# Kernel tuning notes

Hardware: AMD Instinct MI355X
Metric: run time of the kernel (lower is better)

The kernel has to match this reference:

```python
import jax, jax.numpy as jnp
import numpy as np

N = 50000        # nodes
E = 800000       # edges (before self loops)
F_IN = 128
HID = 32         # per-head out channels (hidden_size)
H = 4            # heads
NCLS = 10
NG = 64          # graphs in batch
SLOPE = 0.2      # GATConv default negative_slope


def setup_inputs() -> dict:
    key = jax.random.key(0)
    ks = jax.random.split(key, 32)

    def p(k, shape, fan_in):
        s = 1.0 / np.sqrt(fan_in)
        return jax.random.uniform(k, shape, jnp.float32, -s, s)

    inp = {
        'x': jax.random.normal(ks[0], (N, F_IN), jnp.float32),
        'edge_index': jax.random.randint(ks[1], (2, E), 0, N),
        'batch': jnp.sort(jax.random.randint(ks[2], (N,), 0, NG)),
        'enc1_w': p(ks[3], (F_IN, 128), F_IN), 'enc1_b': p(ks[4], (128,), F_IN),
        'enc2_w': p(ks[5], (128, 256), 128),   'enc2_b': p(ks[6], (256,), 128),
        'lin1_w': p(ks[7], (HID, NCLS), HID),  'lin1_b': p(ks[8], (NCLS,), HID),
    }
    dims_in = [256, HID, HID, HID]
    for i in range(4):
        kk = jax.random.split(ks[9 + i], 4)
        din = dims_in[i]
        inp[f'g{i+1}_w'] = p(kk[0], (din, H * HID), din)
        inp[f'g{i+1}_as'] = p(kk[1], (H, HID), HID)
        inp[f'g{i+1}_ad'] = p(kk[2], (H, HID), HID)
        inp[f'g{i+1}_b'] = p(kk[3], (HID,), HID)
    return inp


def gat_layer(h_in, w, a_s, a_d, b, src, dst):
    # h: [N,H,C] per-head projected features
    h = (h_in @ w).reshape(N, H, HID)
    sc_s = jnp.sum(h * a_s, axis=-1)                 # [N,H] att_src . x
    sc_d = jnp.sum(h * a_d, axis=-1)                 # [N,H] att_dst . x
    e = jax.nn.leaky_relu(sc_s[src] + sc_d[dst], SLOPE)   # [Etot,H]
    m = jax.ops.segment_max(e, dst, num_segments=N)
    m = jnp.where(jnp.isfinite(m), m, 0.0)
    al = jnp.exp(e - m[dst])
    den = jax.ops.segment_sum(al, dst, num_segments=N)
    al = al / jnp.maximum(den[dst], 1e-16)           # segment softmax over in-edges
    msg = h[src] * al[:, :, None]                    # [Etot,H,C]
    out = jax.ops.segment_sum(msg, dst, num_segments=N)  # [N,H,C]
    return out.mean(axis=1) + b                      # concat=False -> head mean + bias


def reference(x, edge_index, batch,
              enc1_w, enc1_b, enc2_w, enc2_b, lin1_w, lin1_b,
              g1_w, g1_as, g1_ad, g1_b,
              g2_w, g2_as, g2_ad, g2_b,
              g3_w, g3_as, g3_ad, g3_b,
              g4_w, g4_as, g4_ad, g4_b):
    loops = jnp.arange(N)
    src = jnp.concatenate([edge_index[0], loops])    # PyG add_self_loops=True
    dst = jnp.concatenate([edge_index[1], loops])
    h = x @ enc1_w + enc1_b                          # no activation in original
    h = h @ enc2_w + enc2_b
    h = jax.nn.elu(gat_layer(h, g1_w, g1_as, g1_ad, g1_b, src, dst))
    h = jax.nn.elu(gat_layer(h, g2_w, g2_as, g2_ad, g2_b, src, dst))
    h = jax.nn.elu(gat_layer(h, g3_w, g3_as, g3_ad, g3_b, src, dst))
    h = jax.nn.elu(gat_layer(h, g4_w, g4_as, g4_ad, g4_b, src, dst))
    sums = jax.ops.segment_sum(h, batch, num_segments=NG)
    cnt = jax.ops.segment_sum(jnp.ones((N,), h.dtype), batch, num_segments=NG)
    pooled = sums / jnp.maximum(cnt, 1.0)[:, None]   # global_mean_pool
    return pooled @ lin1_w + lin1_b                  # dropout off at inference
```

## Files before the change

kernel.cpp:

```cpp
#include <hip/hip_runtime.h>
#include <hip/hip_fp16.h>
#include <math.h>

#define NNODES 50000
#define NEDGES 800000
#define ETOT   (NEDGES + NNODES)
#define HIDC   32
#define NGRAPH 64
#define NCLS   10
#define SLOPE  0.2f
#define SCAN_BLOCKS ((NNODES + 255) / 256)

typedef _Float16 h8 __attribute__((ext_vector_type(8)));
typedef float f32x4 __attribute__((ext_vector_type(4)));

__device__ __forceinline__ float lrelu(float v) { return v > 0.f ? v : SLOPE * v; }

__global__ void hist_kernel(const int* __restrict__ ei, int* __restrict__ deg,
                            int* __restrict__ epos) {
  int base = blockIdx.x * 1024 + threadIdx.x;
  #pragma unroll
  for (int u = 0; u < 4; ++u) {
    int e = base + u * 256;
    if (e < NEDGES) {
      int d = ei[NEDGES + e];
      epos[e] = atomicAdd(&deg[d], 1);
    }
  }
}

__global__ __launch_bounds__(256)
void scan_block_kernel(const int* __restrict__ deg, int* __restrict__ row_start,
                       int* __restrict__ bsum) {
  __shared__ int wsum[4];
  int i = blockIdx.x * 256 + threadIdx.x;
  int v = (i < NNODES) ? (deg[i] + 1) : 0;
  int lane = threadIdx.x & 63, w = threadIdx.x >> 6;
  int x = v;
  #pragma unroll
  for (int d = 1; d < 64; d <<= 1) {
    int y = __shfl_up(x, d);
    if (lane >= d) x += y;
  }
  if (lane == 63) wsum[w] = x;
  __syncthreads();
  int woff = 0;
  #pragma unroll
  for (int j = 0; j < 4; ++j) if (j < w) woff += wsum[j];
  int incl = x + woff;
  if (i < NNODES) row_start[i] = incl - v;
  if (threadIdx.x == 255) bsum[blockIdx.x] = incl;
}

__global__ __launch_bounds__(256)
void scan_add_kernel(const int* __restrict__ bsum, int* __restrict__ row_start,
                     int* __restrict__ col_src) {
  __shared__ int wsum[4];
  int tid = threadIdx.x;
  int v = (tid < blockIdx.x) ? bsum[tid] : 0;
  int lane = tid & 63, w = tid >> 6;
  #pragma unroll
  for (int d = 32; d >= 1; d >>= 1) v += __shfl_xor(v, d);
  if (lane == 0) wsum[w] = v;
  __syncthreads();
  int boff = wsum[0] + wsum[1] + wsum[2] + wsum[3];
  int i = blockIdx.x * 256 + tid;
  if (i < NNODES) {
    int rs = row_start[i] + boff;
    row_start[i] = rs;
    col_src[rs] = i;
  }
  if (i == 0) row_start[NNODES] = ETOT;
}

__global__ void scatter_kernel(const int* __restrict__ ei, const int* __restrict__ row_start,
                               const int* __restrict__ epos, int* __restrict__ col_src) {
  int base = blockIdx.x * 1024 + threadIdx.x;
  #pragma unroll
  for (int u = 0; u < 4; ++u) {
    int e = base + u * 256;
    if (e < NEDGES) {
      int s = ei[e], d = ei[NEDGES + e];
      col_src[row_start[d] + 1 + epos[e]] = s;
    }
  }
}

__device__ void gemm_tile(const float* __restrict__ A, const float* __restrict__ B,
                          float* __restrict__ C, int K, int N, int row0, int col0,
                          float (*As)[68], float (*Bs)[68]) {
  int tid = threadIdx.x;
  int tx = tid & 15, ty = tid >> 4;
  float acc[4][4] = {};
  for (int k0 = 0; k0 < K; k0 += 32) {
    #pragma unroll
    for (int i = 0; i < 8; ++i) {
      int idx = tid + i * 256;
      int r = idx >> 5, c = idx & 31;
      As[c][r] = A[(size_t)(row0 + r) * K + k0 + c];
    }
    #pragma unroll
    for (int i = 0; i < 8; ++i) {
      int idx = tid + i * 256;
      int r = idx >> 6, c = idx & 63;
      Bs[r][c] = B[(size_t)(k0 + r) * N + col0 + c];
    }
    __syncthreads();
    #pragma unroll
    for (int k = 0; k < 32; ++k) {
      float a4[4], b4[4];
      #pragma unroll
      for (int i = 0; i < 4; ++i) a4[i] = As[k][ty * 4 + i];
      #pragma unroll
      for (int j = 0; j < 4; ++j) b4[j] = Bs[k][tx * 4 + j];
      #pragma unroll
      for (int i = 0; i < 4; ++i)
        #pragma unroll
        for (int j = 0; j < 4; ++j)
          acc[i][j] = fmaf(a4[i], b4[j], acc[i][j]);
    }
    __syncthreads();
  }
  #pragma unroll
  for (int i = 0; i < 4; ++i)
    #pragma unroll
    for (int j = 0; j < 4; ++j)
      C[(size_t)(row0 + ty * 4 + i) * N + col0 + tx * 4 + j] = acc[i][j];
}

__global__ __launch_bounds__(256)
void wprep1(const float* __restrict__ enc1_w, const float* __restrict__ enc2_w,
            const float* __restrict__ enc1_b, const float* __restrict__ enc2_b,
            const float* __restrict__ gw1, const float* __restrict__ gas1, const float* __restrict__ gad1,
            const float* __restrict__ gw2, const float* __restrict__ gas2, const float* __restrict__ gad2,
            const float* __restrict__ gw3, const float* __restrict__ gas3, const float* __restrict__ gad3,
            float* __restrict__ T1, float* __restrict__ b2c,
            float* __restrict__ Ws2, float* __restrict__ Ws3, float* __restrict__ Ws4,
            float* __restrict__ pooled) {
  __shared__ float As[32][68];
  __shared__ float Bs[32][68];
  int b = blockIdx.x, tid = threadIdx.x;
  if (b < 8) {
    gemm_tile(enc1_w, enc2_w, T1, 128, 256, (b >> 2) * 64, (b & 3) * 64, As, Bs);
  } else if (b == 8) {
    float acc = enc2_b[tid];
    for (int k = 0; k < 128; ++k) acc = fmaf(enc1_b[k], enc2_w[k * 256 + tid], acc);
    b2c[tid] = acc;
    for (int i = tid; i < NGRAPH * HIDC + NGRAPH; i += 256) pooled[i] = 0.f;
  } else {
    const float* W   = (b == 9) ? gw1  : (b == 10) ? gw2  : gw3;
    const float* as_ = (b == 9) ? gas1 : (b == 10) ? gas2 : gas3;
    const float* ad_ = (b == 9) ? gad1 : (b == 10) ? gad2 : gad3;
    float* Ws        = (b == 9) ? Ws2  : (b == 10) ? Ws3  : Ws4;
    int r = tid >> 3, j = tid & 7, h = j & 3;
    const float* a = (j < 4) ? as_ : ad_;
    float s = 0.f;
    for (int c = 0; c < 32; ++c) s = fmaf(W[r * 128 + h * 32 + c], a[h * 32 + c], s);
    Ws[tid] = s;
  }
}

__global__ __launch_bounds__(256)
void wprep2(const float* __restrict__ T1, const float* __restrict__ gw0,
            const float* __restrict__ b2c, float* __restrict__ Wc, float* __restrict__ bc) {
  __shared__ float As[32][68];
  __shared__ float Bs[32][68];
  int b = blockIdx.x, tid = threadIdx.x;
  if (b < 4) {
    gemm_tile(T1, gw0, Wc, 256, 128, (b >> 1) * 64, (b & 1) * 64, As, Bs);
  } else if (tid < 128) {
    float acc = 0.f;
    for (int k = 0; k < 256; ++k) acc = fmaf(b2c[k], gw0[k * 128 + tid], acc);
    bc[tid] = acc;
  }
}

__global__ __launch_bounds__(256)
void wprep3(const float* __restrict__ Wc, const float* __restrict__ gas0,
            const float* __restrict__ gad0, const float* __restrict__ bc,
            _Float16* __restrict__ WT, float* __restrict__ soff1) {
  int b = blockIdx.x, tid = threadIdx.x;
  if (b < 8) {
    #pragma unroll
    for (int i = 0; i < 8; ++i) {
      int t = b * 2048 + i * 256 + tid;
      int c = t >> 7, k = t & 127;
      WT[t] = (_Float16)Wc[k * 128 + c];
    }
  } else {
    for (int idx = tid; idx < 1024; idx += 256) {
      int j = idx >> 7, k = idx & 127, h = j & 3;
      const float* a = (j < 4) ? gas0 : gad0;
      float s = 0.f;
      for (int c = 0; c < 32; ++c) s = fmaf(Wc[k * 128 + h * 32 + c], a[h * 32 + c], s);
      WT[(size_t)(128 + j) * 128 + k] = (_Float16)s;
    }
    for (int idx = tid; idx < 1024; idx += 256)
      WT[(size_t)136 * 128 + idx] = (_Float16)0.f;
    if (tid < 8) {
      int h = tid & 3;
      const float* a = (tid < 4) ? gas0 : gad0;
      float s = 0.f;
      for (int c = 0; c < 32; ++c) s = fmaf(bc[h * 32 + c], a[h * 32 + c], s);
      soff1[tid] = s;
    }
  }
}

__global__ void wprep4(const float* __restrict__ gw1, const float* __restrict__ gw2,
                       const float* __restrict__ gw3, _Float16* __restrict__ WT2) {
  int b = blockIdx.x, tid = threadIdx.x;
  const float* W = (b == 0) ? gw1 : (b == 1) ? gw2 : gw3;
  for (int i = tid; i < 4096; i += 256) {
    int c = i >> 7, kh = i & 127, k = kh >> 2, h = kh & 3;
    WT2[b * 4096 + i] = (_Float16)(W[k * 128 + h * 32 + c] * 0.25f);
  }
}

__global__ __launch_bounds__(256)
void gemm_mfma(const float* __restrict__ x, const _Float16* __restrict__ WT,
               const float* __restrict__ bc, const float* __restrict__ soff,
               __half* __restrict__ hproj_h,
               float* __restrict__ scs, float* __restrict__ scd) {
  __shared__ _Float16 Ash[64][32];
  int tid = threadIdx.x, wave = tid >> 6, lane = tid & 63;
  int row0 = blockIdx.x * 64;
  f32x4 acc[9] = {};

  int r = tid >> 2;
  int kg = (tid & 3) * 8;
  #pragma unroll 1
  for (int ks = 0; ks < 4; ++ks) {
    float4 v0 = make_float4(0.f, 0.f, 0.f, 0.f), v1 = v0;
    int grow = row0 + r;
    if (grow < NNODES) {
      const float4* xp = (const float4*)(x + (size_t)grow * 128 + ks * 32 + kg);
      v0 = xp[0]; v1 = xp[1];
    }
    __syncthreads();
    h8 hv;
    hv[0] = (_Float16)v0.x; hv[1] = (_Float16)v0.y;
    hv[2] = (_Float16)v0.z; hv[3] = (_Float16)v0.w;
    hv[4] = (_Float16)v1.x; hv[5] = (_Float16)v1.y;
    hv[6] = (_Float16)v1.z; hv[7] = (_Float16)v1.w;
    *(h8*)&Ash[r][kg] = hv;
    __syncthreads();
    h8 af = *(const h8*)&Ash[(wave << 4) + (lane & 15)][(lane >> 4) * 8];
    #pragma unroll
    for (int ct = 0; ct < 9; ++ct) {
      h8 bf = *(const h8*)(WT + (size_t)(ct * 16 + (lane & 15)) * 128 + ks * 32 + (lane >> 4) * 8);
      acc[ct] = __builtin_amdgcn_mfma_f32_16x16x32_f16(af, bf, acc[ct], 0, 0, 0);
    }
  }
  int colL = lane & 15;
  int rbase = row0 + (wave << 4) + ((lane >> 4) << 2);
  #pragma unroll
  for (int reg = 0; reg < 4; ++reg) {
    int node = rbase + reg;
    if (node >= NNODES) continue;
    #pragma unroll
    for (int ct = 0; ct < 8; ++ct) {
      int c = ct * 16 + colL;
      float v = acc[ct][reg] + bc[c];
      hproj_h[(size_t)node * 128 + c] = __float2half_rn(v);
    }
    float sv = acc[8][reg];
    if (colL < 4)      scs[(size_t)node * 4 + colL]     = sv + soff[colL];
    else if (colL < 8) scd[(size_t)node * 4 + colL - 4] = sv + soff[colL];
  }
}

__global__ __launch_bounds__(256)
void gat_edge_kernel(const __half2* __restrict__ hproj_h,
                     const float* __restrict__ scs, const float* __restrict__ scd,
                     const int* __restrict__ row_start, const int* __restrict__ col_src,
                     const float* __restrict__ bias, float* __restrict__ hout,
                     __half* __restrict__ hout_h) {
  __shared__ int src_sh[4][64];
  __shared__ __align__(16) float al_sh[4][256];
  int wave = threadIdx.x >> 6, lane = threadIdx.x & 63;
  int half = lane >> 5, l32 = lane & 31;
  int node = blockIdx.x * 8 + wave * 2 + half;
  bool nvalid = node < NNODES;
  int s = 0, deg = 0;
  if (nvalid) {
    s = row_start[node];
    deg = row_start[node + 1] - s;
  }
  int dmax = max(deg, __shfl_xor(deg, 32));
  float4 sd = nvalid ? *(const float4*)(scd + (size_t)node * 4)
                     : make_float4(0.f, 0.f, 0.f, 0.f);

  int g2 = l32 >> 4;
  int r  = l32 & 15;
  int head = r >> 2;
  const uint4* hp4 = (const uint4*)hproj_h;

  float den = 0.f;
  float acc[8] = {};
  int nchunks = (dmax + 31) >> 5;
  for (int ch = 0; ch < nchunks; ++ch) {
    int ebase = ch * 32;
    int eidx = ebase + l32;
    bool valid = nvalid && (eidx < deg);
    int srcv = 0;
    float4 ss = make_float4(0.f, 0.f, 0.f, 0.f);
    if (valid) {
      srcv = col_src[s + eidx];
      ss = *(const float4*)(scs + (size_t)srcv * 4);
    }
    float a0 = valid ? __expf(lrelu(ss.x + sd.x)) : 0.f;
    float a1 = valid ? __expf(lrelu(ss.y + sd.y)) : 0.f;
    float a2 = valid ? __expf(lrelu(ss.z + sd.z)) : 0.f;
    float a3 = valid ? __expf(lrelu(ss.w + sd.w)) : 0.f;
    src_sh[wave][lane] = srcv;
    *(float4*)&al_sh[wave][lane * 4] = make_float4(a0, a1, a2, a3);
    int cnt = min(32, dmax - ebase);
    int ngc = (cnt + 1) >> 1;
    #pragma unroll 2
    for (int jg = 0; jg < ngc; ++jg) {
      int slot = half * 32 + jg * 2 + g2;
      int src = src_sh[wave][slot];
      float al = al_sh[wave][slot * 4 + head];
      den += al;
      uint4 p = hp4[(size_t)src * 16 + r];
      float2 f0 = __half22float2(*(__half2*)&p.x);
      float2 f1 = __half22float2(*(__half2*)&p.y);
      float2 f2 = __half22float2(*(__half2*)&p.z);
      float2 f3 = __half22float2(*(__half2*)&p.w);
      acc[0] = fmaf(al, f0.x, acc[0]); acc[1] = fmaf(al, f0.y, acc[1]);
      acc[2] = fmaf(al, f1.x, acc[2]); acc[3] = fmaf(al, f1.y, acc[3]);
      acc[4] = fmaf(al, f2.x, acc[4]); acc[5] = fmaf(al, f2.y, acc[5]);
      acc[6] = fmaf(al, f3.x, acc[6]); acc[7] = fmaf(al, f3.y, acc[7]);
    }
  }
  den += __shfl_xor(den, 16);
  float rd = 1.f / fmaxf(den, 1e-16f);
  #pragma unroll
  for (int k = 0; k < 8; ++k) acc[k] *= rd;
  #pragma unroll
  for (int k = 0; k < 8; ++k) acc[k] += __shfl_xor(acc[k], 16);
  #pragma unroll
  for (int k = 0; k < 8; ++k) acc[k] += __shfl_xor(acc[k], 4);
  #pragma unroll
  for (int k = 0; k < 8; ++k) acc[k] += __shfl_xor(acc[k], 8);
  if (nvalid && l32 < 4) {
    float o[8];
    #pragma unroll
    for (int k = 0; k < 8; ++k) {
      float v = acc[k] * 0.25f + bias[8 * l32 + k];
      o[k] = v > 0.f ? v : expm1f(v);
    }
    float* op = hout + (size_t)node * 32 + 8 * l32;
    *(float4*)op       = make_float4(o[0], o[1], o[2], o[3]);
    *(float4*)(op + 4) = make_float4(o[4], o[5], o[6], o[7]);
    __half2 hp[4];
    hp[0] = __floats2half2_rn(o[0], o[1]);
    hp[1] = __floats2half2_rn(o[2], o[3]);
    hp[2] = __floats2half2_rn(o[4], o[5]);
    hp[3] = __floats2half2_rn(o[6], o[7]);
    *(uint4*)(hout_h + (size_t)node * 32 + 8 * l32) = *(uint4*)hp;
  }
}

__global__ __launch_bounds__(256)
void scores32(const float* __restrict__ h, const float* __restrict__ Ws,
              float* __restrict__ scs, float* __restrict__ scd) {
  __shared__ float ws[8][36];
  int tid = threadIdx.x;
  if (tid < 256) ws[tid & 7][tid >> 3] = Ws[tid];
  __syncthreads();
  int wave = tid >> 6, lane = tid & 63;
  int node = blockIdx.x * 4 + wave;
  if (node >= NNODES) return;
  float x = (lane < 32) ? h[(size_t)node * 32 + lane] : 0.f;
  float acc[8];
  #pragma unroll
  for (int j = 0; j < 8; ++j) acc[j] = x * ws[j][lane & 31];
  #pragma unroll
  for (int d = 32; d >= 1; d >>= 1)
    #pragma unroll
    for (int j = 0; j < 8; ++j) acc[j] += __shfl_xor(acc[j], d);
  if (lane == 0) {
    *(float4*)(scs + (size_t)node * 4) = make_float4(acc[0], acc[1], acc[2], acc[3]);
    *(float4*)(scd + (size_t)node * 4) = make_float4(acc[4], acc[5], acc[6], acc[7]);
  }
}

__global__ __launch_bounds__(256)
void gat_agg_kernel(const __half2* __restrict__ hin_h,
                    const float* __restrict__ scs, const float* __restrict__ scd,
                    const int* __restrict__ row_start, const int* __restrict__ col_src,
                    float* __restrict__ agg) {
  __shared__ int src_sh[4][64];
  __shared__ __align__(16) float al_sh[4][256];
  int wave = threadIdx.x >> 6, lane = threadIdx.x & 63;
  int half = lane >> 5, l32 = lane & 31;
  int node = blockIdx.x * 8 + wave * 2 + half;
  bool nvalid = node < NNODES;
  int s = 0, deg = 0;
  if (nvalid) {
    s = row_start[node];
    deg = row_start[node + 1] - s;
  }
  int dmax = max(deg, __shfl_xor(deg, 32));
  float4 sd = nvalid ? *(const float4*)(scd + (size_t)node * 4)
                     : make_float4(0.f, 0.f, 0.f, 0.f);

  int g2 = l32 >> 4;
  int r  = l32 & 15;
  float den0 = 0.f, den1 = 0.f, den2 = 0.f, den3 = 0.f;
  float acc[8] = {};
  int nchunks = (dmax + 31) >> 5;
  for (int ch = 0; ch < nchunks; ++ch) {
    int ebase = ch * 32;
    int eidx = ebase + l32;
    bool valid = nvalid && (eidx < deg);
    int srcv = 0;
    float4 ss = make_float4(0.f, 0.f, 0.f, 0.f);
    if (valid) {
      srcv = col_src[s + eidx];
      ss = *(const float4*)(scs + (size_t)srcv * 4);
    }
    float a0 = valid ? __expf(lrelu(ss.x + sd.x)) : 0.f;
    float a1 = valid ? __expf(lrelu(ss.y + sd.y)) : 0.f;
    float a2 = valid ? __expf(lrelu(ss.z + sd.z)) : 0.f;
    float a3 = valid ? __expf(lrelu(ss.w + sd.w)) : 0.f;
    src_sh[wave][lane] = srcv;
    *(float4*)&al_sh[wave][lane * 4] = make_float4(a0, a1, a2, a3);
    int cnt = min(32, dmax - ebase);
    int ngc = (cnt + 1) >> 1;
    #pragma unroll 2
    for (int jg = 0; jg < ngc; ++jg) {
      int slot = half * 32 + jg * 2 + g2;
      int src = src_sh[wave][slot];
      float4 al = *(float4*)&al_sh[wave][slot * 4];
      float2 f = __half22float2(hin_h[(size_t)src * 16 + r]);
      den0 += al.x; den1 += al.y; den2 += al.z; den3 += al.w;
      acc[0] = fmaf(al.x, f.x, acc[0]); acc[1] = fmaf(al.x, f.y, acc[1]);
      acc[2] = fmaf(al.y, f.x, acc[2]); acc[3] = fmaf(al.y, f.y, acc[3]);
      acc[4] = fmaf(al.z, f.x, acc[4]); acc[5] = fmaf(al.z, f.y, acc[5]);
      acc[6] = fmaf(al.w, f.x, acc[6]); acc[7] = fmaf(al.w, f.y, acc[7]);
    }
  }
  #pragma unroll
  for (int k = 0; k < 8; ++k) acc[k] += __shfl_xor(acc[k], 16);
  den0 += __shfl_xor(den0, 16); den1 += __shfl_xor(den1, 16);
  den2 += __shfl_xor(den2, 16); den3 += __shfl_xor(den3, 16);
  float r0 = 1.f / fmaxf(den0, 1e-16f), r1 = 1.f / fmaxf(den1, 1e-16f);
  float r2 = 1.f / fmaxf(den2, 1e-16f), r3 = 1.f / fmaxf(den3, 1e-16f);
  acc[0] *= r0; acc[1] *= r0; acc[2] *= r1; acc[3] *= r1;
  acc[4] *= r2; acc[5] *= r2; acc[6] *= r3; acc[7] *= r3;
  if (nvalid && g2 == 0) {
    float4* ap = (float4*)(agg + (size_t)node * 128 + r * 8);
    ap[0] = make_float4(acc[0], acc[2], acc[4], acc[6]);
    ap[1] = make_float4(acc[1], acc[3], acc[5], acc[7]);
  }
}

__global__ __launch_bounds__(256)
void post_proj_mfma(const float* __restrict__ agg,
                    const _Float16* __restrict__ WT2,
                    const float* __restrict__ bias,
                    const float* __restrict__ Ws,
                    __half* __restrict__ hout_h,
                    float* __restrict__ scs, float* __restrict__ scd,
                    float* __restrict__ hout32) {
  __shared__ _Float16 Ash[64][32];
  __shared__ float o_lds[64][33];
  __shared__ float WsS[32][8];
  int tid = threadIdx.x, wave = tid >> 6, lane = tid & 63;
  int row0 = blockIdx.x * 64;
  f32x4 acc[2] = {};
  if (Ws) WsS[tid >> 3][tid & 7] = Ws[tid];

  int r = tid >> 2;
  int kg = (tid & 3) * 8;
  #pragma unroll 1
  for (int ks = 0; ks < 4; ++ks) {
    float4 v0 = make_float4(0.f, 0.f, 0.f, 0.f), v1 = v0;
    int grow = row0 + r;
    if (grow < NNODES) {
      const float4* xp = (const float4*)(agg + (size_t)grow * 128 + ks * 32 + kg);
      v0 = xp[0]; v1 = xp[1];
    }
    __syncthreads();
    h8 hv;
    hv[0] = (_Float16)v0.x; hv[1] = (_Float16)v0.y;
    hv[2] = (_Float16)v0.z; hv[3] = (_Float16)v0.w;
    hv[4] = (_Float16)v1.x; hv[5] = (_Float16)v1.y;
    hv[6] = (_Float16)v1.z; hv[7] = (_Float16)v1.w;
    *(h8*)&Ash[r][kg] = hv;
    __syncthreads();
    h8 af = *(const h8*)&Ash[(wave << 4) + (lane & 15)][(lane >> 4) * 8];
    #pragma unroll
    for (int ct = 0; ct < 2; ++ct) {
      h8 bf = *(const h8*)(WT2 + (size_t)(ct * 16 + (lane & 15)) * 128 + ks * 32 + (lane >> 4) * 8);
      acc[ct] = __builtin_amdgcn_mfma_f32_16x16x32_f16(af, bf, acc[ct], 0, 0, 0);
    }
  }
  int colL = lane & 15;
  int rloc = (wave << 4) + ((lane >> 4) << 2);
  #pragma unroll
  for (int reg = 0; reg < 4; ++reg) {
    int node = row0 + rloc + reg;
    #pragma unroll
    for (int ct = 0; ct < 2; ++ct) {
      int c = ct * 16 + colL;
      float v = acc[ct][reg] + bias[c];
      float o = v > 0.f ? v : expm1f(v);
      o_lds[rloc + reg][c] = o;
      if (node < NNODES) {
        if (hout_h) hout_h[(size_t)node * 32 + c] = __float2half_rn(o);
        if (hout32) hout32[(size_t)node * 32 + c] = o;
      }
    }
  }
  if (Ws) {
    __syncthreads();
    #pragma unroll
    for (int t = 0; t < 2; ++t) {
      int idx = tid * 2 + t;
      int nl = idx >> 3, j = idx & 7;
      int node = row0 + nl;
      float sc = 0.f;
      #pragma unroll
      for (int c = 0; c < 32; ++c) sc = fmaf(o_lds[nl][c], WsS[c][j], sc);
      if (node < NNODES) {
        if (j < 4) scs[(size_t)node * 4 + j] = sc;
        else       scd[(size_t)node * 4 + j - 4] = sc;
      }
    }
  }
}

#define POOL_BLOCKS 128
__global__ __launch_bounds__(256)
void pool_kernel(const float* __restrict__ h, const int* __restrict__ batch,
                 float* __restrict__ pooled, float* __restrict__ cnt) {
  __shared__ float acc[NGRAPH][HIDC];
  __shared__ float ccnt[NGRAPH];
  int tid = threadIdx.x;
  const int chunk = (NNODES + POOL_BLOCKS - 1) / POOL_BLOCKS;
  int n0 = blockIdx.x * chunk;
  int n1 = min(n0 + chunk, NNODES);
  if (n0 >= NNODES) return;
  int g0 = batch[n0], g1 = batch[n1 - 1];
  int rows = g1 - g0 + 1;
  for (int idx = tid; idx < rows * HIDC; idx += 256)
    acc[g0 + (idx >> 5)][idx & 31] = 0.f;
  for (int g = tid; g < rows; g += 256) ccnt[g0 + g] = 0.f;
  __syncthreads();
  int c = tid & 31;
  for (int node = n0 + (tid >> 5); node < n1; node += 8) {
    int g = batch[node];
    atomicAdd(&acc[g][c], h[(size_t)node * HIDC + c]);
    if (c == 0) atomicAdd(&ccnt[g], 1.f);
  }
  __syncthreads();
  for (int idx = tid; idx < rows * HIDC; idx += 256) {
    int g = g0 + (idx >> 5), cc = idx & 31;
    atomicAdd(&pooled[g * HIDC + cc], acc[g][cc]);
  }
  for (int g = tid; g < rows; g += 256) atomicAdd(&cnt[g0 + g], ccnt[g0 + g]);
}

__global__ void final_kernel(const float* __restrict__ pooled, const float* __restrict__ cnt,
                             const float* __restrict__ w, const float* __restrict__ b,
                             float* __restrict__ out) {
  int t = threadIdx.x;
  if (t >= NGRAPH * NCLS) return;
  int g = t / NCLS, j = t - g * NCLS;
  float inv = 1.f / fmaxf(cnt[g], 1.f);
  float acc = 0.f;
  #pragma unroll
  for (int c = 0; c < HIDC; ++c)
    acc = fmaf(pooled[g * HIDC + c], w[c * NCLS + j], acc);
  out[t] = acc * inv + b[j];
}

extern "C" void kernel_launch(void* const* d_in, const int* in_sizes, int n_in,
                              void* d_out, int out_size, void* d_ws, size_t ws_size,
                              hipStream_t stream) {
  const float* x      = (const float*)d_in[0];
  const int*   ei     = (const int*)d_in[1];
  const int*   batch  = (const int*)d_in[2];
  const float* enc1_w = (const float*)d_in[3];
  const float* enc1_b = (const float*)d_in[4];
  const float* enc2_w = (const float*)d_in[5];
  const float* enc2_b = (const float*)d_in[6];
  const float* lin1_w = (const float*)d_in[7];
  const float* lin1_b = (const float*)d_in[8];
  const float* gw[4]  = {(const float*)d_in[9],  (const float*)d_in[13], (const float*)d_in[17], (const float*)d_in[21]};
  const float* gas[4] = {(const float*)d_in[10], (const float*)d_in[14], (const float*)d_in[18], (const float*)d_in[22]};
  const float* gad[4] = {(const float*)d_in[11], (const float*)d_in[15], (const float*)d_in[19], (const float*)d_in[23]};
  const float* gb[4]  = {(const float*)d_in[12], (const float*)d_in[16], (const float*)d_in[20], (const float*)d_in[24]};
  float* out = (float*)d_out;

  __half* hproj_h   = (__half*)d_ws;
  _Float16* WT      = (_Float16*)(hproj_h + (size_t)NNODES * 128);
  _Float16* WT2     = WT + 144 * 128;
  __half* hsm_h     = (__half*)(WT2 + 3 * 4096);
  float*  fws       = (float*)(hsm_h + (size_t)NNODES * 32);
  float* hsmall = fws;
  float* agg    = hsmall + (size_t)NNODES * 32;
  float* scs    = agg    + (size_t)NNODES * 128;
  float* scd    = scs    + (size_t)NNODES * 4;
  float* pooled = scd    + (size_t)NNODES * 4;
  float* cnt    = pooled + NGRAPH * HIDC;
  float* T1     = cnt + NGRAPH;
  float* Wc     = T1 + 128 * 256;
  float* b2c    = Wc + 128 * 128;
  float* bc     = b2c + 256;
  float* soff1  = bc + 128;
  float* Ws2    = soff1 + 8;
  float* Ws3    = Ws2 + 32 * 8;
  float* Ws4    = Ws3 + 32 * 8;
  int* deg       = (int*)(Ws4 + 32 * 8);
  int* row_start = deg + NNODES;
  int* col_src   = row_start + NNODES + 1;
  int* epos      = col_src + ETOT;
  int* bsum      = epos + NEDGES;

  hipMemsetAsync(deg, 0, NNODES * sizeof(int), stream);
  hist_kernel<<<(NEDGES + 1023) / 1024, 256, 0, stream>>>(ei, deg, epos);
  scan_block_kernel<<<SCAN_BLOCKS, 256, 0, stream>>>(deg, row_start, bsum);
  scan_add_kernel<<<SCAN_BLOCKS, 256, 0, stream>>>(bsum, row_start, col_src);
  scatter_kernel<<<(NEDGES + 1023) / 1024, 256, 0, stream>>>(ei, row_start, epos, col_src);

  wprep1<<<12, 256, 0, stream>>>(enc1_w, enc2_w, enc1_b, enc2_b,
                                 gw[1], gas[1], gad[1], gw[2], gas[2], gad[2],
                                 gw[3], gas[3], gad[3],
                                 T1, b2c, Ws2, Ws3, Ws4, pooled);
  wprep2<<<5, 256, 0, stream>>>(T1, gw[0], b2c, Wc, bc);
  wprep3<<<9, 256, 0, stream>>>(Wc, gas[0], gad[0], bc, WT, soff1);
  wprep4<<<3, 256, 0, stream>>>(gw[1], gw[2], gw[3], WT2);

  int nodeblocks64 = (NNODES + 63) / 64;
  int edgeblocks = (NNODES + 7) / 8;

  gemm_mfma<<<nodeblocks64, 256, 0, stream>>>(x, WT, bc, soff1, hproj_h, scs, scd);
  gat_edge_kernel<<<edgeblocks, 256, 0, stream>>>((const __half2*)hproj_h, scs, scd,
                                                  row_start, col_src, gb[0], hsmall, hsm_h);
  scores32<<<(NNODES + 3) / 4, 256, 0, stream>>>(hsmall, Ws2, scs, scd);

  gat_agg_kernel<<<edgeblocks, 256, 0, stream>>>((const __half2*)hsm_h, scs, scd, row_start, col_src, agg);
  post_proj_mfma<<<nodeblocks64, 256, 0, stream>>>(agg, WT2,            gb[1], Ws3, hsm_h, scs, scd, nullptr);

  gat_agg_kernel<<<edgeblocks, 256, 0, stream>>>((const __half2*)hsm_h, scs, scd, row_start, col_src, agg);
  post_proj_mfma<<<nodeblocks64, 256, 0, stream>>>(agg, WT2 + 4096,     gb[2], Ws4, hsm_h, scs, scd, nullptr);

  gat_agg_kernel<<<edgeblocks, 256, 0, stream>>>((const __half2*)hsm_h, scs, scd, row_start, col_src, agg);
  post_proj_mfma<<<nodeblocks64, 256, 0, stream>>>(agg, WT2 + 8192,     gb[3], nullptr, nullptr, nullptr, nullptr, hsmall);

  pool_kernel<<<POOL_BLOCKS, 256, 0, stream>>>(hsmall, batch, pooled, cnt);
  final_kernel<<<1, 640, 0, stream>>>(pooled, cnt, lin1_w, lin1_b, out);
}
```

Measured before the change: 322.9 us.

## Fuse GAT aggregation with post-projection MFMA, ping-pong feature buffers

```diff
diff --git a/kernel.cpp b/kernel.cpp
--- a/kernel.cpp
+++ b/kernel.cpp
@@ -388,126 +388,109 @@
 }
 
 __global__ __launch_bounds__(256)
-void gat_agg_kernel(const __half2* __restrict__ hin_h,
-                    const float* __restrict__ scs, const float* __restrict__ scd,
-                    const int* __restrict__ row_start, const int* __restrict__ col_src,
-                    float* __restrict__ agg) {
+void fused_gat_layer(const __half2* __restrict__ hin_h,
+                     const float* __restrict__ scs, const float* __restrict__ scd,
+                     const int* __restrict__ row_start, const int* __restrict__ col_src,
+                     const _Float16* __restrict__ WT2, const float* __restrict__ bias,
+                     const float* __restrict__ Ws,
+                     __half* __restrict__ hout_h,
+                     float* __restrict__ scs_out, float* __restrict__ scd_out,
+                     float* __restrict__ hout32) {
+  __shared__ _Float16 agg_h[64][136];
   __shared__ int src_sh[4][64];
   __shared__ __align__(16) float al_sh[4][256];
-  int wave = threadIdx.x >> 6, lane = threadIdx.x & 63;
-  int half = lane >> 5, l32 = lane & 31;
-  int node = blockIdx.x * 8 + wave * 2 + half;
-  bool nvalid = node < NNODES;
-  int s = 0, deg = 0;
-  if (nvalid) {
-    s = row_start[node];
-    deg = row_start[node + 1] - s;
-  }
-  int dmax = max(deg, __shfl_xor(deg, 32));
-  float4 sd = nvalid ? *(const float4*)(scd + (size_t)node * 4)
-                     : make_float4(0.f, 0.f, 0.f, 0.f);
-
-  int g2 = l32 >> 4;
-  int r  = l32 & 15;
-  float den0 = 0.f, den1 = 0.f, den2 = 0.f, den3 = 0.f;
-  float acc[8] = {};
-  int nchunks = (dmax + 31) >> 5;
-  for (int ch = 0; ch < nchunks; ++ch) {
-    int ebase = ch * 32;
-    int eidx = ebase + l32;
-    bool valid = nvalid && (eidx < deg);
-    int srcv = 0;
-    float4 ss = make_float4(0.f, 0.f, 0.f, 0.f);
-    if (valid) {
-      srcv = col_src[s + eidx];
-      ss = *(const float4*)(scs + (size_t)srcv * 4);
-    }
-    float a0 = valid ? __expf(lrelu(ss.x + sd.x)) : 0.f;
-    float a1 = valid ? __expf(lrelu(ss.y + sd.y)) : 0.f;
-    float a2 = valid ? __expf(lrelu(ss.z + sd.z)) : 0.f;
-    float a3 = valid ? __expf(lrelu(ss.w + sd.w)) : 0.f;
-    src_sh[wave][lane] = srcv;
-    *(float4*)&al_sh[wave][lane * 4] = make_float4(a0, a1, a2, a3);
-    int cnt = min(32, dmax - ebase);
-    int ngc = (cnt + 1) >> 1;
-    #pragma unroll 2
-    for (int jg = 0; jg < ngc; ++jg) {
-      int slot = half * 32 + jg * 2 + g2;
-      int src = src_sh[wave][slot];
-      float4 al = *(float4*)&al_sh[wave][slot * 4];
-      float2 f = __half22float2(hin_h[(size_t)src * 16 + r]);
-      den0 += al.x; den1 += al.y; den2 += al.z; den3 += al.w;
-      acc[0] = fmaf(al.x, f.x, acc[0]); acc[1] = fmaf(al.x, f.y, acc[1]);
-      acc[2] = fmaf(al.y, f.x, acc[2]); acc[3] = fmaf(al.y, f.y, acc[3]);
-      acc[4] = fmaf(al.z, f.x, acc[4]); acc[5] = fmaf(al.z, f.y, acc[5]);
-      acc[6] = fmaf(al.w, f.x, acc[6]); acc[7] = fmaf(al.w, f.y, acc[7]);
-    }
-  }
-  #pragma unroll
-  for (int k = 0; k < 8; ++k) acc[k] += __shfl_xor(acc[k], 16);
-  den0 += __shfl_xor(den0, 16); den1 += __shfl_xor(den1, 16);
-  den2 += __shfl_xor(den2, 16); den3 += __shfl_xor(den3, 16);
-  float r0 = 1.f / fmaxf(den0, 1e-16f), r1 = 1.f / fmaxf(den1, 1e-16f);
-  float r2 = 1.f / fmaxf(den2, 1e-16f), r3 = 1.f / fmaxf(den3, 1e-16f);
-  acc[0] *= r0; acc[1] *= r0; acc[2] *= r1; acc[3] *= r1;
-  acc[4] *= r2; acc[5] *= r2; acc[6] *= r3; acc[7] *= r3;
-  if (nvalid && g2 == 0) {
-    float4* ap = (float4*)(agg + (size_t)node * 128 + r * 8);
-    ap[0] = make_float4(acc[0], acc[2], acc[4], acc[6]);
-    ap[1] = make_float4(acc[1], acc[3], acc[5], acc[7]);
-  }
-}
-
-__global__ __launch_bounds__(256)
-void post_proj_mfma(const float* __restrict__ agg,
-                    const _Float16* __restrict__ WT2,
-                    const float* __restrict__ bias,
-                    const float* __restrict__ Ws,
-                    __half* __restrict__ hout_h,
-                    float* __restrict__ scs, float* __restrict__ scd,
-                    float* __restrict__ hout32) {
-  __shared__ _Float16 Ash[64][32];
   __shared__ float o_lds[64][33];
   __shared__ float WsS[32][8];
   int tid = threadIdx.x, wave = tid >> 6, lane = tid & 63;
-  int row0 = blockIdx.x * 64;
-  f32x4 acc[2] = {};
+  int half = lane >> 5, l32 = lane & 31;
+  int n0 = blockIdx.x * 64;
   if (Ws) WsS[tid >> 3][tid & 7] = Ws[tid];
 
-  int r = tid >> 2;
-  int kg = (tid & 3) * 8;
+  int g2 = l32 >> 4;
+  int r  = l32 & 15;
   #pragma unroll 1
+  for (int pi = 0; pi < 8; ++pi) {
+    int nlBase = (wave << 4) + pi * 2;
+    int node = n0 + nlBase + half;
+    bool nvalid = node < NNODES;
+    int s = 0, deg = 0;
+    if (nvalid) {
+      s = row_start[node];
+      deg = row_start[node + 1] - s;
+    }
+    int dmax = max(deg, __shfl_xor(deg, 32));
+    float4 sd = nvalid ? *(const float4*)(scd + (size_t)node * 4)
+                       : make_float4(0.f, 0.f, 0.f, 0.f);
+    float den0 = 0.f, den1 = 0.f, den2 = 0.f, den3 = 0.f;
+    float acc[8] = {};
+    int nchunks = (dmax + 31) >> 5;
+    for (int ch = 0; ch < nchunks; ++ch) {
+      int ebase = ch * 32;
+      int eidx = ebase + l32;
+      bool valid = nvalid && (eidx < deg);
+      int srcv = 0;
+      float4 ss = make_float4(0.f, 0.f, 0.f, 0.f);
+      if (valid) {
+        srcv = col_src[s + eidx];
+        ss = *(const float4*)(scs + (size_t)srcv * 4);
+      }
+      float a0 = valid ? __expf(lrelu(ss.x + sd.x)) : 0.f;
+      float a1 = valid ? __expf(lrelu(ss.y + sd.y)) : 0.f;
+      float a2 = valid ? __expf(lrelu(ss.z + sd.z)) : 0.f;
+      float a3 = valid ? __expf(lrelu(ss.w + sd.w)) : 0.f;
+      src_sh[wave][lane] = srcv;
+      *(float4*)&al_sh[wave][lane * 4] = make_float4(a0, a1, a2, a3);
+      int cnt = min(32, dmax - ebase);
+      int ngc = (cnt + 1) >> 1;
+      #pragma unroll 2
+      for (int jg = 0; jg < ngc; ++jg) {
+        int slot = half * 32 + jg * 2 + g2;
+        int src = src_sh[wave][slot];
+        float4 al = *(float4*)&al_sh[wave][slot * 4];
+        float2 f = __half22float2(hin_h[(size_t)src * 16 + r]);
+        den0 += al.x; den1 += al.y; den2 += al.z; den3 += al.w;
+        acc[0] = fmaf(al.x, f.x, acc[0]); acc[1] = fmaf(al.x, f.y, acc[1]);
+        acc[2] = fmaf(al.y, f.x, acc[2]); acc[3] = fmaf(al.y, f.y, acc[3]);
+        acc[4] = fmaf(al.z, f.x, acc[4]); acc[5] = fmaf(al.z, f.y, acc[5]);
+        acc[6] = fmaf(al.w, f.x, acc[6]); acc[7] = fmaf(al.w, f.y, acc[7]);
+      }
+    }
+    #pragma unroll
+    for (int k = 0; k < 8; ++k) acc[k] += __shfl_xor(acc[k], 16);
+    den0 += __shfl_xor(den0, 16); den1 += __shfl_xor(den1, 16);
+    den2 += __shfl_xor(den2, 16); den3 += __shfl_xor(den3, 16);
+    float r0 = 1.f / fmaxf(den0, 1e-16f), r1 = 1.f / fmaxf(den1, 1e-16f);
+    float r2 = 1.f / fmaxf(den2, 1e-16f), r3 = 1.f / fmaxf(den3, 1e-16f);
+    if (g2 == 0) {
+      h8 hv;
+      hv[0] = (_Float16)(acc[0] * r0); hv[1] = (_Float16)(acc[2] * r1);
+      hv[2] = (_Float16)(acc[4] * r2); hv[3] = (_Float16)(acc[6] * r3);
+      hv[4] = (_Float16)(acc[1] * r0); hv[5] = (_Float16)(acc[3] * r1);
+      hv[6] = (_Float16)(acc[5] * r2); hv[7] = (_Float16)(acc[7] * r3);
+      *(h8*)&agg_h[nlBase + half][8 * r] = hv;
+    }
+  }
+  __syncthreads();
+
+  f32x4 pacc[2] = {};
+  #pragma unroll
   for (int ks = 0; ks < 4; ++ks) {
-    float4 v0 = make_float4(0.f, 0.f, 0.f, 0.f), v1 = v0;
-    int grow = row0 + r;
-    if (grow < NNODES) {
-      const float4* xp = (const float4*)(agg + (size_t)grow * 128 + ks * 32 + kg);
-      v0 = xp[0]; v1 = xp[1];
-    }
-    __syncthreads();
-    h8 hv;
-    hv[0] = (_Float16)v0.x; hv[1] = (_Float16)v0.y;
-    hv[2] = (_Float16)v0.z; hv[3] = (_Float16)v0.w;
-    hv[4] = (_Float16)v1.x; hv[5] = (_Float16)v1.y;
-    hv[6] = (_Float16)v1.z; hv[7] = (_Float16)v1.w;
-    *(h8*)&Ash[r][kg] = hv;
-    __syncthreads();
-    h8 af = *(const h8*)&Ash[(wave << 4) + (lane & 15)][(lane >> 4) * 8];
+    h8 af = *(const h8*)&agg_h[(wave << 4) + (lane & 15)][ks * 32 + (lane >> 4) * 8];
     #pragma unroll
     for (int ct = 0; ct < 2; ++ct) {
       h8 bf = *(const h8*)(WT2 + (size_t)(ct * 16 + (lane & 15)) * 128 + ks * 32 + (lane >> 4) * 8);
-      acc[ct] = __builtin_amdgcn_mfma_f32_16x16x32_f16(af, bf, acc[ct], 0, 0, 0);
+      pacc[ct] = __builtin_amdgcn_mfma_f32_16x16x32_f16(af, bf, pacc[ct], 0, 0, 0);
     }
   }
   int colL = lane & 15;
   int rloc = (wave << 4) + ((lane >> 4) << 2);
   #pragma unroll
   for (int reg = 0; reg < 4; ++reg) {
-    int node = row0 + rloc + reg;
+    int node = n0 + rloc + reg;
     #pragma unroll
     for (int ct = 0; ct < 2; ++ct) {
       int c = ct * 16 + colL;
-      float v = acc[ct][reg] + bias[c];
+      float v = pacc[ct][reg] + bias[c];
       float o = v > 0.f ? v : expm1f(v);
       o_lds[rloc + reg][c] = o;
       if (node < NNODES) {
@@ -522,13 +505,13 @@
     for (int t = 0; t < 2; ++t) {
       int idx = tid * 2 + t;
       int nl = idx >> 3, j = idx & 7;
-      int node = row0 + nl;
+      int node = n0 + nl;
       float sc = 0.f;
       #pragma unroll
       for (int c = 0; c < 32; ++c) sc = fmaf(o_lds[nl][c], WsS[c][j], sc);
       if (node < NNODES) {
-        if (j < 4) scs[(size_t)node * 4 + j] = sc;
-        else       scd[(size_t)node * 4 + j - 4] = sc;
+        if (j < 4) scs_out[(size_t)node * 4 + j] = sc;
+        else       scd_out[(size_t)node * 4 + j - 4] = sc;
       }
     }
   }
@@ -600,13 +583,15 @@
   __half* hproj_h   = (__half*)d_ws;
   _Float16* WT      = (_Float16*)(hproj_h + (size_t)NNODES * 128);
   _Float16* WT2     = WT + 144 * 128;
-  __half* hsm_h     = (__half*)(WT2 + 3 * 4096);
-  float*  fws       = (float*)(hsm_h + (size_t)NNODES * 32);
+  __half* hsm_a     = (__half*)(WT2 + 3 * 4096);
+  __half* hsm_b     = hsm_a + (size_t)NNODES * 32;
+  float*  fws       = (float*)(hsm_b + (size_t)NNODES * 32);
   float* hsmall = fws;
-  float* agg    = hsmall + (size_t)NNODES * 32;
-  float* scs    = agg    + (size_t)NNODES * 128;
-  float* scd    = scs    + (size_t)NNODES * 4;
-  float* pooled = scd    + (size_t)NNODES * 4;
+  float* scs_a  = hsmall + (size_t)NNODES * 32;
+  float* scd_a  = scs_a  + (size_t)NNODES * 4;
+  float* scs_b  = scd_a  + (size_t)NNODES * 4;
+  float* scd_b  = scs_b  + (size_t)NNODES * 4;
+  float* pooled = scd_b  + (size_t)NNODES * 4;
   float* cnt    = pooled + NGRAPH * HIDC;
   float* T1     = cnt + NGRAPH;
   float* Wc     = T1 + 128 * 256;
@@ -639,19 +624,17 @@
   int nodeblocks64 = (NNODES + 63) / 64;
   int edgeblocks = (NNODES + 7) / 8;
 
-  gemm_mfma<<<nodeblocks64, 256, 0, stream>>>(x, WT, bc, soff1, hproj_h, scs, scd);
-  gat_edge_kernel<<<edgeblocks, 256, 0, stream>>>((const __half2*)hproj_h, scs, scd,
-                                                  row_start, col_src, gb[0], hsmall, hsm_h);
-  scores32<<<(NNODES + 3) / 4, 256, 0, stream>>>(hsmall, Ws2, scs, scd);
-
-  gat_agg_kernel<<<edgeblocks, 256, 0, stream>>>((const __half2*)hsm_h, scs, scd, row_start, col_src, agg);
-  post_proj_mfma<<<nodeblocks64, 256, 0, stream>>>(agg, WT2,            gb[1], Ws3, hsm_h, scs, scd, nullptr);
-
-  gat_agg_kernel<<<edgeblocks, 256, 0, stream>>>((const __half2*)hsm_h, scs, scd, row_start, col_src, agg);
-  post_proj_mfma<<<nodeblocks64, 256, 0, stream>>>(agg, WT2 + 4096,     gb[2], Ws4, hsm_h, scs, scd, nullptr);
-
-  gat_agg_kernel<<<edgeblocks, 256, 0, stream>>>((const __half2*)hsm_h, scs, scd, row_start, col_src, agg);
-  post_proj_mfma<<<nodeblocks64, 256, 0, stream>>>(agg, WT2 + 8192,     gb[3], nullptr, nullptr, nullptr, nullptr, hsmall);
+  gemm_mfma<<<nodeblocks64, 256, 0, stream>>>(x, WT, bc, soff1, hproj_h, scs_a, scd_a);
+  gat_edge_kernel<<<edgeblocks, 256, 0, stream>>>((const __half2*)hproj_h, scs_a, scd_a,
+                                                  row_start, col_src, gb[0], hsmall, hsm_a);
+  scores32<<<(NNODES + 3) / 4, 256, 0, stream>>>(hsmall, Ws2, scs_a, scd_a);
+
+  fused_gat_layer<<<nodeblocks64, 256, 0, stream>>>((const __half2*)hsm_a, scs_a, scd_a,
+      row_start, col_src, WT2,        gb[1], Ws3, hsm_b, scs_b, scd_b, nullptr);
+  fused_gat_layer<<<nodeblocks64, 256, 0, stream>>>((const __half2*)hsm_b, scs_b, scd_b,
+      row_start, col_src, WT2 + 4096, gb[2], Ws4, hsm_a, scs_a, scd_a, nullptr);
+  fused_gat_layer<<<nodeblocks64, 256, 0, stream>>>((const __half2*)hsm_a, scs_a, scd_a,
+      row_start, col_src, WT2 + 8192, gb[3], nullptr, nullptr, nullptr, nullptr, hsmall);
 
   pool_kernel<<<POOL_BLOCKS, 256, 0, stream>>>(hsmall, batch, pooled, cnt);
   final_kernel<<<1, 640, 0, stream>>>(pooled, cnt, lin1_w, lin1_b, out);
```

Result: slower. 334.2 us (+3.5%).

## Fuse layer-2 score computation into edge kernel and store aggregates as fp16

Applied to the files above, without the earlier changes.

```diff
diff --git a/kernel.cpp b/kernel.cpp
--- a/kernel.cpp
+++ b/kernel.cpp
@@ -274,11 +274,16 @@
 void gat_edge_kernel(const __half2* __restrict__ hproj_h,
                      const float* __restrict__ scs, const float* __restrict__ scd,
                      const int* __restrict__ row_start, const int* __restrict__ col_src,
-                     const float* __restrict__ bias, float* __restrict__ hout,
-                     __half* __restrict__ hout_h) {
+                     const float* __restrict__ bias, const float* __restrict__ Ws,
+                     __half* __restrict__ hout_h,
+                     float* __restrict__ scs_out, float* __restrict__ scd_out) {
   __shared__ int src_sh[4][64];
   __shared__ __align__(16) float al_sh[4][256];
-  int wave = threadIdx.x >> 6, lane = threadIdx.x & 63;
+  __shared__ float WsS[32][8];
+  int tid = threadIdx.x;
+  WsS[tid >> 3][tid & 7] = Ws[tid];
+  __syncthreads();
+  int wave = tid >> 6, lane = tid & 63;
   int half = lane >> 5, l32 = lane & 31;
   int node = blockIdx.x * 8 + wave * 2 + half;
   bool nvalid = node < NNODES;
@@ -351,39 +356,28 @@
       float v = acc[k] * 0.25f + bias[8 * l32 + k];
       o[k] = v > 0.f ? v : expm1f(v);
     }
-    float* op = hout + (size_t)node * 32 + 8 * l32;
-    *(float4*)op       = make_float4(o[0], o[1], o[2], o[3]);
-    *(float4*)(op + 4) = make_float4(o[4], o[5], o[6], o[7]);
     __half2 hp[4];
     hp[0] = __floats2half2_rn(o[0], o[1]);
     hp[1] = __floats2half2_rn(o[2], o[3]);
     hp[2] = __floats2half2_rn(o[4], o[5]);
     hp[3] = __floats2half2_rn(o[6], o[7]);
     *(uint4*)(hout_h + (size_t)node * 32 + 8 * l32) = *(uint4*)hp;
-  }
-}
-
-__global__ __launch_bounds__(256)
-void scores32(const float* __restrict__ h, const float* __restrict__ Ws,
-              float* __restrict__ scs, float* __restrict__ scd) {
-  __shared__ float ws[8][36];
-  int tid = threadIdx.x;
-  if (tid < 256) ws[tid & 7][tid >> 3] = Ws[tid];
-  __syncthreads();
-  int wave = tid >> 6, lane = tid & 63;
-  int node = blockIdx.x * 4 + wave;
-  if (node >= NNODES) return;
-  float x = (lane < 32) ? h[(size_t)node * 32 + lane] : 0.f;
-  float acc[8];
-  #pragma unroll
-  for (int j = 0; j < 8; ++j) acc[j] = x * ws[j][lane & 31];
-  #pragma unroll
-  for (int d = 32; d >= 1; d >>= 1)
-    #pragma unroll
-    for (int j = 0; j < 8; ++j) acc[j] += __shfl_xor(acc[j], d);
-  if (lane == 0) {
-    *(float4*)(scs + (size_t)node * 4) = make_float4(acc[0], acc[1], acc[2], acc[3]);
-    *(float4*)(scd + (size_t)node * 4) = make_float4(acc[4], acc[5], acc[6], acc[7]);
+    float sc[8];
+    #pragma unroll
+    for (int j = 0; j < 8; ++j) {
+      float v = 0.f;
+      #pragma unroll
+      for (int k = 0; k < 8; ++k) v = fmaf(o[k], WsS[8 * l32 + k][j], v);
+      sc[j] = v;
+    }
+    #pragma unroll
+    for (int j = 0; j < 8; ++j) sc[j] += __shfl_xor(sc[j], 1);
+    #pragma unroll
+    for (int j = 0; j < 8; ++j) sc[j] += __shfl_xor(sc[j], 2);
+    if (l32 == 0) {
+      *(float4*)(scs_out + (size_t)node * 4) = make_float4(sc[0], sc[1], sc[2], sc[3]);
+      *(float4*)(scd_out + (size_t)node * 4) = make_float4(sc[4], sc[5], sc[6], sc[7]);
+    }
   }
 }
 
@@ -391,7 +385,7 @@
 void gat_agg_kernel(const __half2* __restrict__ hin_h,
                     const float* __restrict__ scs, const float* __restrict__ scd,
                     const int* __restrict__ row_start, const int* __restrict__ col_src,
-                    float* __restrict__ agg) {
+                    _Float16* __restrict__ agg_h16) {
   __shared__ int src_sh[4][64];
   __shared__ __align__(16) float al_sh[4][256];
   int wave = threadIdx.x >> 6, lane = threadIdx.x & 63;
@@ -449,17 +443,18 @@
   den2 += __shfl_xor(den2, 16); den3 += __shfl_xor(den3, 16);
   float r0 = 1.f / fmaxf(den0, 1e-16f), r1 = 1.f / fmaxf(den1, 1e-16f);
   float r2 = 1.f / fmaxf(den2, 1e-16f), r3 = 1.f / fmaxf(den3, 1e-16f);
-  acc[0] *= r0; acc[1] *= r0; acc[2] *= r1; acc[3] *= r1;
-  acc[4] *= r2; acc[5] *= r2; acc[6] *= r3; acc[7] *= r3;
   if (nvalid && g2 == 0) {
-    float4* ap = (float4*)(agg + (size_t)node * 128 + r * 8);
-    ap[0] = make_float4(acc[0], acc[2], acc[4], acc[6]);
-    ap[1] = make_float4(acc[1], acc[3], acc[5], acc[7]);
-  }
-}
-
-__global__ __launch_bounds__(256)
-void post_proj_mfma(const float* __restrict__ agg,
+    h8 hv;
+    hv[0] = (_Float16)(acc[0] * r0); hv[1] = (_Float16)(acc[2] * r1);
+    hv[2] = (_Float16)(acc[4] * r2); hv[3] = (_Float16)(acc[6] * r3);
+    hv[4] = (_Float16)(acc[1] * r0); hv[5] = (_Float16)(acc[3] * r1);
+    hv[6] = (_Float16)(acc[5] * r2); hv[7] = (_Float16)(acc[7] * r3);
+    *(h8*)(agg_h16 + (size_t)node * 128 + 8 * r) = hv;
+  }
+}
+
+__global__ __launch_bounds__(256)
+void post_proj_mfma(const _Float16* __restrict__ agg_h16,
                     const _Float16* __restrict__ WT2,
                     const float* __restrict__ bias,
                     const float* __restrict__ Ws,
@@ -478,18 +473,11 @@
   int kg = (tid & 3) * 8;
   #pragma unroll 1
   for (int ks = 0; ks < 4; ++ks) {
-    float4 v0 = make_float4(0.f, 0.f, 0.f, 0.f), v1 = v0;
+    h8 hv = {};
     int grow = row0 + r;
-    if (grow < NNODES) {
-      const float4* xp = (const float4*)(agg + (size_t)grow * 128 + ks * 32 + kg);
-      v0 = xp[0]; v1 = xp[1];
-    }
+    if (grow < NNODES)
+      hv = *(const h8*)(agg_h16 + (size_t)grow * 128 + ks * 32 + kg);
     __syncthreads();
-    h8 hv;
-    hv[0] = (_Float16)v0.x; hv[1] = (_Float16)v0.y;
-    hv[2] = (_Float16)v0.z; hv[3] = (_Float16)v0.w;
-    hv[4] = (_Float16)v1.x; hv[5] = (_Float16)v1.y;
-    hv[6] = (_Float16)v1.z; hv[7] = (_Float16)v1.w;
     *(h8*)&Ash[r][kg] = hv;
     __syncthreads();
     h8 af = *(const h8*)&Ash[(wave << 4) + (lane & 15)][(lane >> 4) * 8];
@@ -601,12 +589,14 @@
   _Float16* WT      = (_Float16*)(hproj_h + (size_t)NNODES * 128);
   _Float16* WT2     = WT + 144 * 128;
   __half* hsm_h     = (__half*)(WT2 + 3 * 4096);
-  float*  fws       = (float*)(hsm_h + (size_t)NNODES * 32);
+  _Float16* agg_h16 = (_Float16*)(hsm_h + (size_t)NNODES * 32);
+  float*  fws       = (float*)(agg_h16 + (size_t)NNODES * 128);
   float* hsmall = fws;
-  float* agg    = hsmall + (size_t)NNODES * 32;
-  float* scs    = agg    + (size_t)NNODES * 128;
-  float* scd    = scs    + (size_t)NNODES * 4;
-  float* pooled = scd    + (size_t)NNODES * 4;
+  float* scs_a  = hsmall + (size_t)NNODES * 32;
+  float* scd_a  = scs_a  + (size_t)NNODES * 4;
+  float* scs_b  = scd_a  + (size_t)NNODES * 4;
+  float* scd_b  = scs_b  + (size_t)NNODES * 4;
+  float* pooled = scd_b  + (size_t)NNODES * 4;
   float* cnt    = pooled + NGRAPH * HIDC;
   float* T1     = cnt + NGRAPH;
   float* Wc     = T1 + 128 * 256;
@@ -639,19 +629,19 @@
   int nodeblocks64 = (NNODES + 63) / 64;
   int edgeblocks = (NNODES + 7) / 8;
 
-  gemm_mfma<<<nodeblocks64, 256, 0, stream>>>(x, WT, bc, soff1, hproj_h, scs, scd);
-  gat_edge_kernel<<<edgeblocks, 256, 0, stream>>>((const __half2*)hproj_h, scs, scd,
-                                                  row_start, col_src, gb[0], hsmall, hsm_h);
-  scores32<<<(NNODES + 3) / 4, 256, 0, stream>>>(hsmall, Ws2, scs, scd);
-
-  gat_agg_kernel<<<edgeblocks, 256, 0, stream>>>((const __half2*)hsm_h, scs, scd, row_start, col_src, agg);
-  post_proj_mfma<<<nodeblocks64, 256, 0, stream>>>(agg, WT2,            gb[1], Ws3, hsm_h, scs, scd, nullptr);
-
-  gat_agg_kernel<<<edgeblocks, 256, 0, stream>>>((const __half2*)hsm_h, scs, scd, row_start, col_src, agg);
-  post_proj_mfma<<<nodeblocks64, 256, 0, stream>>>(agg, WT2 + 4096,     gb[2], Ws4, hsm_h, scs, scd, nullptr);
-
-  gat_agg_kernel<<<edgeblocks, 256, 0, stream>>>((const __half2*)hsm_h, scs, scd, row_start, col_src, agg);
-  post_proj_mfma<<<nodeblocks64, 256, 0, stream>>>(agg, WT2 + 8192,     gb[3], nullptr, nullptr, nullptr, nullptr, hsmall);
+  gemm_mfma<<<nodeblocks64, 256, 0, stream>>>(x, WT, bc, soff1, hproj_h, scs_a, scd_a);
+  gat_edge_kernel<<<edgeblocks, 256, 0, stream>>>((const __half2*)hproj_h, scs_a, scd_a,
+                                                  row_start, col_src, gb[0], Ws2,
+                                                  hsm_h, scs_b, scd_b);
+
+  gat_agg_kernel<<<edgeblocks, 256, 0, stream>>>((const __half2*)hsm_h, scs_b, scd_b, row_start, col_src, agg_h16);
+  post_proj_mfma<<<nodeblocks64, 256, 0, stream>>>(agg_h16, WT2,        gb[1], Ws3, hsm_h, scs_a, scd_a, nullptr);
+
+  gat_agg_kernel<<<edgeblocks, 256, 0, stream>>>((const __half2*)hsm_h, scs_a, scd_a, row_start, col_src, agg_h16);
+  post_proj_mfma<<<nodeblocks64, 256, 0, stream>>>(agg_h16, WT2 + 4096, gb[2], Ws4, hsm_h, scs_b, scd_b, nullptr);
+
+  gat_agg_kernel<<<edgeblocks, 256, 0, stream>>>((const __half2*)hsm_h, scs_b, scd_b, row_start, col_src, agg_h16);
+  post_proj_mfma<<<nodeblocks64, 256, 0, stream>>>(agg_h16, WT2 + 8192, gb[3], nullptr, nullptr, nullptr, nullptr, hsmall);
 
   pool_kernel<<<POOL_BLOCKS, 256, 0, stream>>>(hsmall, batch, pooled, cnt);
   final_kernel<<<1, 640, 0, stream>>>(pooled, cnt, lin1_w, lin1_b, out);
```

Measured after the change: 297.7 us. -7.8%, faster.
